# Kernel tuning notes

Measured on AMD Instinct MI355X. Metric: run time of the kernel, lower is better.

Reference implementation:

```python
import jax, jax.numpy as jnp
import numpy as np

B = 16384          # tokens
H = 2048           # hidden_size
E = 8              # num_experts
K = 2              # top-k
HF = H // 4        # expert bottleneck dim


def setup_inputs() -> dict:
    key = jax.random.key(0)
    k0, k1, k2, k3 = jax.random.split(key, 4)
    scale = lambda kk, shape, fan: jax.random.normal(kk, shape, jnp.float32) * (1.0 / np.sqrt(fan))
    x = jax.random.normal(k0, (B, H), jnp.float32)
    W1 = scale(k1, (E, H, HF), H)      # experts[e][0].weight (transposed)
    b1 = jnp.zeros((E, HF), jnp.float32)
    W2 = scale(k2, (E, HF), HF)        # experts[e][2].weight (out dim 1, no bias)
    Wg = scale(k3, (H, E), H)          # gate.weight (transposed)
    bg = jnp.zeros((E,), jnp.float32)
    return {"x": x, "W1": W1, "b1": b1, "W2": W2, "Wg": Wg, "bg": bg}


def reference(x, W1, b1, W2, Wg, bg):
    # Gating (eval mode: no noise branch)
    logits = x @ Wg + bg                                  # [B, E]
    top_w, top_i = jax.lax.top_k(logits, K)               # [B, K]
    w = jax.nn.softmax(top_w, axis=-1)                    # [B, K]
    # Scatter top-k softmax weights into dense combine weights [B, E];
    # unselected experts get weight 0, so the dense all-expert compute
    # below is mathematically identical to the masked dispatch loop.
    combine = jnp.zeros_like(logits).at[jnp.arange(x.shape[0])[:, None], top_i].add(w)
    # All-expert MLP: Linear -> exact GELU -> Linear(->1, no bias)
    h = jax.nn.gelu(jnp.einsum('bh,ehf->bef', x, W1) + b1, approximate=False)  # [B, E, HF]
    o = jnp.einsum('bef,ef->be', h, W2)                   # [B, E]
    final_scores = jnp.sum(combine * o, axis=-1, keepdims=True)  # [B, 1]
    return final_scores, logits
```

## Files before the change

### kernel.cpp

```cpp
#include <hip/hip_runtime.h>
#include <math.h>

#define B_TOK 16384
#define H_DIM 2048
#define NE    8
#define TOPK  2
#define HFD   512

#define BK 64
#define NKSTEP (H_DIM / BK)
#define PTMAX 129
#define PROWS 33792

static constexpr size_t OFF_COUNTS = 0;
static constexpr size_t OFF_CBASE  = 128;
static constexpr size_t OFF_BUCKET = 1024;
static constexpr size_t OFF_WSLOT  = 525312;
static constexpr size_t OFF_ROUTE  = 656384;
static constexpr size_t OFF_INV    = 721920;
static constexpr size_t OFF_WGT    = 1u << 20;
static constexpr size_t OFF_P4     = 1572864;
static constexpr size_t OFF_W1Q    = 4u << 20;
static constexpr size_t OFF_XB     = 20971520;

typedef short bfrag __attribute__((ext_vector_type(8)));
typedef float facc  __attribute__((ext_vector_type(16)));

__device__ inline unsigned short f2bf(float f) {
    union { float f; unsigned u; } v; v.f = f;
    unsigned r = v.u + 0x7FFFu + ((v.u >> 16) & 1u);
    return (unsigned short)(r >> 16);
}
__device__ inline unsigned pack2(float lo, float hi) {
    return (unsigned)f2bf(lo) | ((unsigned)f2bf(hi) << 16);
}

__device__ __forceinline__ void gload_lds16(const void* g, void* l) {
    __builtin_amdgcn_global_load_lds(
        (const __attribute__((address_space(1))) unsigned int*)g,
        (__attribute__((address_space(3))) unsigned int*)l, 16, 0, 0);
}

__global__ __launch_bounds__(256)
void wg_transpose_kernel(const float* __restrict__ Wg,
                         float* __restrict__ WgT)
{
    const int t = threadIdx.x;
    #pragma unroll
    for (int rep = 0; rep < H_DIM / 256; ++rep) {
        const int h = rep * 256 + t;
        const float4 a = *reinterpret_cast<const float4*>(Wg + (size_t)h * NE);
        const float4 b = *reinterpret_cast<const float4*>(Wg + (size_t)h * NE + 4);
        #pragma unroll
        for (int rr = 0; rr < 8; ++rr) {
            float* W = WgT + (size_t)rr * (NE * H_DIM);
            W[0 * H_DIM + h] = a.x;  W[1 * H_DIM + h] = a.y;
            W[2 * H_DIM + h] = a.z;  W[3 * H_DIM + h] = a.w;
            W[4 * H_DIM + h] = b.x;  W[5 * H_DIM + h] = b.y;
            W[6 * H_DIM + h] = b.z;  W[7 * H_DIM + h] = b.w;
        }
    }
}

__global__ __launch_bounds__(256)
void prep_w1_kernel(const float* __restrict__ W1,
                    unsigned short* __restrict__ W1q)
{
    const int e     = blockIdx.x >> 5;
    const int kstep = blockIdx.x & 31;
    const int tid   = threadIdx.x;

    const float* src = W1 + ((size_t)e * H_DIM + kstep * BK) * HFD;

    #pragma unroll
    for (int slot = 0; slot < 8; ++slot) {
        #pragma unroll
        for (int half = 0; half < 2; ++half) {
            const int f  = half * 256 + tid;
            const int fq = f >> 7;
            const int fl = f & 127;
            float v[8];
            #pragma unroll
            for (int j = 0; j < 8; ++j)
                v[j] = src[(size_t)(slot * 8 + j) * HFD + f];
            uint4 p;
            p.x = pack2(v[0], v[1]); p.y = pack2(v[2], v[3]);
            p.z = pack2(v[4], v[5]); p.w = pack2(v[6], v[7]);
            *reinterpret_cast<uint4*>(
                W1q + ((size_t)((e * 4 + fq) * 32 + kstep)) * 8192
                    + (slot * 128 + fl) * 8) = p;
        }
    }
}

__global__ __launch_bounds__(256)
void gate_logits_kernel(const float* __restrict__ x,
                        const float* __restrict__ WgT,
                        const float* __restrict__ bg,
                        float* __restrict__ out_logits,
                        float* __restrict__ wslot,
                        int*   __restrict__ route,
                        unsigned short* __restrict__ xb)
{
    __shared__ float Wlds[NE * H_DIM];

    const int tid = threadIdx.x;
    const float* Wsrc = WgT + (size_t)(blockIdx.x & 7) * (NE * H_DIM);
    #pragma unroll
    for (int i = 0; i < (NE * H_DIM) / (256 * 4); ++i) {
        const int idx = (i * 256 + tid) * 4;
        *reinterpret_cast<float4*>(&Wlds[idx]) =
            *reinterpret_cast<const float4*>(Wsrc + idx);
    }
    __syncthreads();

    const int w = tid >> 6, l = tid & 63;
    const int tbase = blockIdx.x * 64 + w * 16;

    for (int pass = 0; pass < 4; ++pass) {
        const int t0 = tbase + pass * 4;
        float acc[4][NE];
        #pragma unroll
        for (int j = 0; j < 4; ++j)
            #pragma unroll
            for (int e = 0; e < NE; ++e) acc[j][e] = 0.f;

        for (int i = 0; i < 8; ++i) {
            const int h = i * 256 + 4 * l;
            float4 xv[4];
            #pragma unroll
            for (int j = 0; j < 4; ++j)
                xv[j] = *reinterpret_cast<const float4*>(
                    x + (size_t)(t0 + j) * H_DIM + h);
            #pragma unroll
            for (int j = 0; j < 4; ++j) {
                uint2 pk;
                pk.x = pack2(xv[j].x, xv[j].y);
                pk.y = pack2(xv[j].z, xv[j].w);
                *reinterpret_cast<uint2*>(xb + (size_t)(t0 + j) * H_DIM + h) = pk;
            }
            #pragma unroll
            for (int e = 0; e < NE; ++e) {
                const float4 wv = *reinterpret_cast<const float4*>(&Wlds[e * H_DIM + h]);
                #pragma unroll
                for (int j = 0; j < 4; ++j)
                    acc[j][e] += xv[j].x * wv.x + xv[j].y * wv.y
                               + xv[j].z * wv.z + xv[j].w * wv.w;
            }
        }

        #pragma unroll
        for (int j = 0; j < 4; ++j)
            #pragma unroll
            for (int e = 0; e < NE; ++e)
                #pragma unroll
                for (int off = 32; off > 0; off >>= 1)
                    acc[j][e] += __shfl_xor(acc[j][e], off, 64);

        if (l == 0) {
            #pragma unroll
            for (int j = 0; j < 4; ++j) {
                const int tok = t0 + j;
                float lg[NE];
                #pragma unroll
                for (int e = 0; e < NE; ++e) lg[e] = acc[j][e] + bg[e];

                float4* lo = reinterpret_cast<float4*>(out_logits + (size_t)tok * NE);
                lo[0] = make_float4(lg[0], lg[1], lg[2], lg[3]);
                lo[1] = make_float4(lg[4], lg[5], lg[6], lg[7]);

                int i0 = 0; float v0 = lg[0];
                #pragma unroll
                for (int e = 1; e < NE; ++e)
                    if (lg[e] > v0) { v0 = lg[e]; i0 = e; }
                int i1 = -1; float v1 = -3.4e38f;
                #pragma unroll
                for (int e = 0; e < NE; ++e)
                    if (e != i0 && lg[e] > v1) { v1 = lg[e]; i1 = e; }

                const float w0 = 1.f / (1.f + expf(v1 - v0));
                wslot[tok * 2]     = w0;
                wslot[tok * 2 + 1] = 1.f - w0;
                route[tok] = i0 | (i1 << 8);
            }
        }
    }
}

__global__ __launch_bounds__(1024)
void route_kernel(const int* __restrict__ route,
                  int* __restrict__ counts,
                  int* __restrict__ bucket)
{
    __shared__ int lcnt[NE];
    __shared__ int lbase[NE];
    const int tid = threadIdx.x;
    const int tok = blockIdx.x * 1024 + tid;

    if (tid < NE) lcnt[tid] = 0;
    __syncthreads();

    const int rt = route[tok];
    const int i0 = rt & 255;
    const int i1 = rt >> 8;
    const int r0 = atomicAdd(&lcnt[i0], 1);
    const int r1 = atomicAdd(&lcnt[i1], 1);
    __syncthreads();

    if (tid < NE) lbase[tid] = atomicAdd(&counts[tid], lcnt[tid]);
    __syncthreads();

    bucket[i0 * B_TOK + lbase[i0] + r0] = tok * 2;
    bucket[i1 * B_TOK + lbase[i1] + r1] = tok * 2 + 1;
}

__global__ void prefix_kernel(const int* __restrict__ counts,
                              int* __restrict__ cbase)
{
    if (threadIdx.x == 0 && blockIdx.x == 0) {
        int acc = 0;
        for (int e = 0; e < NE; ++e) {
            const int cp = ((counts[e] + 127) >> 7) << 7;
            cbase[e]      = acc;
            cbase[NE + e] = cp;
            acc += cp;
        }
    }
}

__global__ __launch_bounds__(256)
void invfill_kernel(const int* __restrict__ bucket,
                    const int* __restrict__ counts,
                    const int* __restrict__ cbase,
                    int* __restrict__ inv)
{
    const int e   = blockIdx.x & 7;
    const int pos = (blockIdx.x >> 3) * 256 + threadIdx.x;
    if (pos < counts[e]) inv[bucket[e * B_TOK + pos]] = cbase[e] + pos;
}

__global__ __launch_bounds__(256, 4)
void expert_mfma_kernel(const unsigned short* __restrict__ xb,
                        const unsigned short* __restrict__ W1q,
                        const float* __restrict__ b1,
                        const float* __restrict__ W2,
                        const int* __restrict__ counts,
                        const int* __restrict__ cbase,
                        const int* __restrict__ bucket,
                        float* __restrict__ P4)
{
    const int e  = blockIdx.x & 7;
    const int r  = blockIdx.x >> 3;
    const int pt = r % PTMAX;
    const int fq = r / PTMAX;
    const int n  = counts[e];
    const int pos0 = pt * 128;
    if (pos0 >= n) return;
    const int nt = min(128, n - pos0);
    const int cb = cbase[e];

    __shared__ unsigned short Albs[8192];
    __shared__ unsigned short Blds[8192];
    __shared__ float o_part[2][128];

    const int tid = threadIdx.x;
    const int w   = tid >> 6;
    const int l   = tid & 63;
    const int lo5 = l & 31;
    const int hi  = l >> 5;
    const int wm  = w & 1;
    const int wn  = w >> 1;

    const unsigned short* Aimg = W1q + (size_t)((e * 4 + fq) * 32) * 8192;

    const unsigned short* xsrc0, *xsrc1, *xsrc2, *xsrc3;
    {
        const int u0 = 0 * 256 + tid, u1 = 1 * 256 + tid,
                  u2 = 2 * 256 + tid, u3 = 3 * 256 + tid;
        const int r0 = u0 >> 3, r1 = u1 >> 3, r2 = u2 >> 3, r3 = u3 >> 3;
        const int t0 = bucket[e * B_TOK + min(pos0 + r0, n - 1)] >> 1;
        const int t1 = bucket[e * B_TOK + min(pos0 + r1, n - 1)] >> 1;
        const int t2 = bucket[e * B_TOK + min(pos0 + r2, n - 1)] >> 1;
        const int t3 = bucket[e * B_TOK + min(pos0 + r3, n - 1)] >> 1;
        xsrc0 = xb + (size_t)t0 * H_DIM + (((u0 & 7) ^ (r0 & 7)) * 8);
        xsrc1 = xb + (size_t)t1 * H_DIM + (((u1 & 7) ^ (r1 & 7)) * 8);
        xsrc2 = xb + (size_t)t2 * H_DIM + (((u2 & 7) ^ (r2 & 7)) * 8);
        xsrc3 = xb + (size_t)t3 * H_DIM + (((u3 & 7) ^ (r3 & 7)) * 8);
    }

    facc acc00, acc01, acc10, acc11;
    #pragma unroll
    for (int q = 0; q < 16; ++q) {
        acc00[q] = 0.f; acc01[q] = 0.f; acc10[q] = 0.f; acc11[q] = 0.f;
    }

    for (int kk = 0; kk < NKSTEP; ++kk) {
        const unsigned short* as = Aimg + (size_t)kk * 8192;
        {
            const int o0 = (0 * 256 + tid) * 8, o1 = (1 * 256 + tid) * 8;
            const int o2 = (2 * 256 + tid) * 8, o3 = (3 * 256 + tid) * 8;
            gload_lds16(as + o0, Albs + o0);
            gload_lds16(as + o1, Albs + o1);
            gload_lds16(as + o2, Albs + o2);
            gload_lds16(as + o3, Albs + o3);
            gload_lds16(xsrc0 + kk * BK, Blds + o0);
            gload_lds16(xsrc1 + kk * BK, Blds + o1);
            gload_lds16(xsrc2 + kk * BK, Blds + o2);
            gload_lds16(xsrc3 + kk * BK, Blds + o3);
        }
        __syncthreads();

        #pragma unroll
        for (int s = 0; s < 4; ++s) {
            const int slot  = s * 2 + hi;
            const int chunk = slot ^ (lo5 & 7);
            const bfrag a0 = *reinterpret_cast<const bfrag*>(
                &Albs[(slot * 128 + wm * 64 + lo5) * 8]);
            const bfrag a1 = *reinterpret_cast<const bfrag*>(
                &Albs[(slot * 128 + wm * 64 + 32 + lo5) * 8]);
            const bfrag b0 = *reinterpret_cast<const bfrag*>(
                &Blds[((wn * 64 + lo5) * 8 + chunk) * 8]);
            const bfrag b1v = *reinterpret_cast<const bfrag*>(
                &Blds[((wn * 64 + 32 + lo5) * 8 + chunk) * 8]);
            acc00 = __builtin_amdgcn_mfma_f32_32x32x16_bf16(a0, b0,  acc00, 0, 0, 0);
            acc01 = __builtin_amdgcn_mfma_f32_32x32x16_bf16(a0, b1v, acc01, 0, 0, 0);
            acc10 = __builtin_amdgcn_mfma_f32_32x32x16_bf16(a1, b0,  acc10, 0, 0, 0);
            acc11 = __builtin_amdgcn_mfma_f32_32x32x16_bf16(a1, b1v, acc11, 0, 0, 0);
        }
        __syncthreads();
    }

    const float* b1e = b1 + e * HFD + fq * 128;
    const float* W2e = W2 + e * HFD + fq * 128;
    const float kInvSqrt2 = 0.70710678118654752f;

    float po0 = 0.f, po1 = 0.f;
    #pragma unroll
    for (int mb = 0; mb < 2; ++mb) {
        const int base = wm * 64 + mb * 32 + 4 * hi;
        #pragma unroll
        for (int q = 0; q < 16; ++q) {
            const int frow = base + (q & 3) + 8 * (q >> 2);
            const float bv = b1e[frow];
            const float wv = W2e[frow];
            const float h0 = (mb ? acc10[q] : acc00[q]) + bv;
            const float h1 = (mb ? acc11[q] : acc01[q]) + bv;
            po0 += 0.5f * h0 * (1.f + erff(h0 * kInvSqrt2)) * wv;
            po1 += 0.5f * h1 * (1.f + erff(h1 * kInvSqrt2)) * wv;
        }
    }
    po0 += __shfl_xor(po0, 32, 64);
    po1 += __shfl_xor(po1, 32, 64);

    if (hi == 0) {
        o_part[wm][wn * 64 + lo5]      = po0;
        o_part[wm][wn * 64 + 32 + lo5] = po1;
    }
    __syncthreads();

    if (tid < nt)
        P4[(size_t)fq * PROWS + cb + pos0 + tid] =
            o_part[0][tid] + o_part[1][tid];
}

__global__ __launch_bounds__(256)
void combine_kernel(const int* __restrict__ inv,
                    const float* __restrict__ P4,
                    const float* __restrict__ wslot,
                    float* __restrict__ out_scores)
{
    const int t = blockIdx.x * 256 + threadIdx.x;
    if (t >= B_TOK) return;
    const int g0 = inv[2 * t];
    const int g1 = inv[2 * t + 1];
    const float s0 = ((P4[g0] + P4[PROWS + g0]) + P4[2 * PROWS + g0])
                   + P4[3 * PROWS + g0];
    const float s1 = ((P4[g1] + P4[PROWS + g1]) + P4[2 * PROWS + g1])
                   + P4[3 * PROWS + g1];
    out_scores[t] = wslot[2 * t] * s0 + wslot[2 * t + 1] * s1;
}

extern "C" void kernel_launch(void* const* d_in, const int* in_sizes, int n_in,
                              void* d_out, int out_size, void* d_ws, size_t ws_size,
                              hipStream_t stream)
{
    const float* x  = (const float*)d_in[0];
    const float* W1 = (const float*)d_in[1];
    const float* b1 = (const float*)d_in[2];
    const float* W2 = (const float*)d_in[3];
    const float* Wg = (const float*)d_in[4];
    const float* bg = (const float*)d_in[5];

    float* out        = (float*)d_out;
    float* out_scores = out;
    float* out_logits = out + B_TOK;

    char* ws = (char*)d_ws;
    int*            counts = (int*)           (ws + OFF_COUNTS);
    int*            cbase  = (int*)           (ws + OFF_CBASE);
    int*            bucket = (int*)           (ws + OFF_BUCKET);
    float*          wslot  = (float*)         (ws + OFF_WSLOT);
    int*            route  = (int*)           (ws + OFF_ROUTE);
    int*            inv    = (int*)           (ws + OFF_INV);
    float*          WgT    = (float*)         (ws + OFF_WGT);
    float*          P4     = (float*)         (ws + OFF_P4);
    unsigned short* W1q    = (unsigned short*)(ws + OFF_W1Q);
    unsigned short* xb     = (unsigned short*)(ws + OFF_XB);

    hipMemsetAsync(counts, 0, NE * sizeof(int), stream);

    wg_transpose_kernel<<<1, 256, 0, stream>>>(Wg, WgT);

    prep_w1_kernel<<<NE * NKSTEP, 256, 0, stream>>>(W1, W1q);

    gate_logits_kernel<<<B_TOK / 64, 256, 0, stream>>>(x, WgT, bg, out_logits,
                                                       wslot, route, xb);

    route_kernel<<<B_TOK / 1024, 1024, 0, stream>>>(route, counts, bucket);

    prefix_kernel<<<1, 64, 0, stream>>>(counts, cbase);

    invfill_kernel<<<NE * (B_TOK / 256), 256, 0, stream>>>(bucket, counts,
                                                           cbase, inv);

    expert_mfma_kernel<<<NE * 4 * PTMAX, 256, 0, stream>>>(
        xb, W1q, b1, W2, counts, cbase, bucket, P4);

    combine_kernel<<<B_TOK / 256, 256, 0, stream>>>(inv, P4, wslot, out_scores);
}
```

Measured before the change: 250.7 us.

## Enlarge expert GEMM tiles to 256x256 with double-buffered LDS pipeline

The expert MFMA kernel moves from 128-token x 128-feature tiles with 256 threads to 256x256 tiles with 512 threads. The bottleneck dimension is now split into two halves instead of four. The K loop double-buffers A and B in LDS, prefetching the next step while computing the current one, and raises wave priority around the MFMA block. The W1 prep layout, padding to 256, the partial-sum buffer and the combine kernel are updated to match. This is meant to raise operand reuse per loaded byte, halve redundant gathers of x, and hide global-to-LDS latency. The cost is much higher LDS use (about 130KB) and register pressure, giving one block per CU and more padding waste on partial tiles.

Result: slower. 338.7 us (+35.1%).

```diff
diff --git a/kernel.cpp b/kernel.cpp
--- a/kernel.cpp
+++ b/kernel.cpp
@@ -9,8 +9,8 @@
 
 #define BK 64
 #define NKSTEP (H_DIM / BK)
-#define PTMAX 129
-#define PROWS 33792
+#define PT256 64
+#define PROWS 35840
 
 static constexpr size_t OFF_COUNTS = 0;
 static constexpr size_t OFF_CBASE  = 128;
@@ -19,8 +19,8 @@
 static constexpr size_t OFF_ROUTE  = 656384;
 static constexpr size_t OFF_INV    = 721920;
 static constexpr size_t OFF_WGT    = 1u << 20;
-static constexpr size_t OFF_P4     = 1572864;
-static constexpr size_t OFF_W1Q    = 4u << 20;
+static constexpr size_t OFF_P2     = 1572864;
+static constexpr size_t OFF_W1H    = 4u << 20;
 static constexpr size_t OFF_XB     = 20971520;
 
 typedef short bfrag __attribute__((ext_vector_type(8)));
@@ -64,7 +64,7 @@
 
 __global__ __launch_bounds__(256)
 void prep_w1_kernel(const float* __restrict__ W1,
-                    unsigned short* __restrict__ W1q)
+                    unsigned short* __restrict__ W1h)
 {
     const int e     = blockIdx.x >> 5;
     const int kstep = blockIdx.x & 31;
@@ -75,10 +75,8 @@
     #pragma unroll
     for (int slot = 0; slot < 8; ++slot) {
         #pragma unroll
-        for (int half = 0; half < 2; ++half) {
-            const int f  = half * 256 + tid;
-            const int fq = f >> 7;
-            const int fl = f & 127;
+        for (int fn = 0; fn < 2; ++fn) {
+            const int f = fn * 256 + tid;
             float v[8];
             #pragma unroll
             for (int j = 0; j < 8; ++j)
@@ -87,8 +85,8 @@
             p.x = pack2(v[0], v[1]); p.y = pack2(v[2], v[3]);
             p.z = pack2(v[4], v[5]); p.w = pack2(v[6], v[7]);
             *reinterpret_cast<uint4*>(
-                W1q + ((size_t)((e * 4 + fq) * 32 + kstep)) * 8192
-                    + (slot * 128 + fl) * 8) = p;
+                W1h + ((size_t)((e * 2 + fn) * 32 + kstep)) * 16384
+                    + (slot * 256 + tid) * 8) = p;
         }
     }
 }
@@ -220,7 +218,7 @@
     if (threadIdx.x == 0 && blockIdx.x == 0) {
         int acc = 0;
         for (int e = 0; e < NE; ++e) {
-            const int cp = ((counts[e] + 127) >> 7) << 7;
+            const int cp = ((counts[e] + 255) >> 8) << 8;
             cbase[e]      = acc;
             cbase[NE + e] = cp;
             acc += cp;
@@ -239,29 +237,29 @@
     if (pos < counts[e]) inv[bucket[e * B_TOK + pos]] = cbase[e] + pos;
 }
 
-__global__ __launch_bounds__(256, 4)
+__global__ __launch_bounds__(512, 1)
 void expert_mfma_kernel(const unsigned short* __restrict__ xb,
-                        const unsigned short* __restrict__ W1q,
+                        const unsigned short* __restrict__ W1h,
                         const float* __restrict__ b1,
                         const float* __restrict__ W2,
                         const int* __restrict__ counts,
                         const int* __restrict__ cbase,
                         const int* __restrict__ bucket,
-                        float* __restrict__ P4)
+                        float* __restrict__ P2)
 {
     const int e  = blockIdx.x & 7;
     const int r  = blockIdx.x >> 3;
-    const int pt = r % PTMAX;
-    const int fq = r / PTMAX;
+    const int fn = r & 1;
+    const int pt = r >> 1;
     const int n  = counts[e];
-    const int pos0 = pt * 128;
+    const int pos0 = pt * 256;
     if (pos0 >= n) return;
-    const int nt = min(128, n - pos0);
+    const int nt = min(256, n - pos0);
     const int cb = cbase[e];
 
-    __shared__ unsigned short Albs[8192];
-    __shared__ unsigned short Blds[8192];
-    __shared__ float o_part[2][128];
+    __shared__ unsigned short Ab[2][16384];
+    __shared__ unsigned short Bb[2][16384];
+    __shared__ float o_part[2][256];
 
     const int tid = threadIdx.x;
     const int w   = tid >> 6;
@@ -271,80 +269,95 @@
     const int wm  = w & 1;
     const int wn  = w >> 1;
 
-    const unsigned short* Aimg = W1q + (size_t)((e * 4 + fq) * 32) * 8192;
-
-    const unsigned short* xsrc0, *xsrc1, *xsrc2, *xsrc3;
-    {
-        const int u0 = 0 * 256 + tid, u1 = 1 * 256 + tid,
-                  u2 = 2 * 256 + tid, u3 = 3 * 256 + tid;
-        const int r0 = u0 >> 3, r1 = u1 >> 3, r2 = u2 >> 3, r3 = u3 >> 3;
-        const int t0 = bucket[e * B_TOK + min(pos0 + r0, n - 1)] >> 1;
-        const int t1 = bucket[e * B_TOK + min(pos0 + r1, n - 1)] >> 1;
-        const int t2 = bucket[e * B_TOK + min(pos0 + r2, n - 1)] >> 1;
-        const int t3 = bucket[e * B_TOK + min(pos0 + r3, n - 1)] >> 1;
-        xsrc0 = xb + (size_t)t0 * H_DIM + (((u0 & 7) ^ (r0 & 7)) * 8);
-        xsrc1 = xb + (size_t)t1 * H_DIM + (((u1 & 7) ^ (r1 & 7)) * 8);
-        xsrc2 = xb + (size_t)t2 * H_DIM + (((u2 & 7) ^ (r2 & 7)) * 8);
-        xsrc3 = xb + (size_t)t3 * H_DIM + (((u3 & 7) ^ (r3 & 7)) * 8);
-    }
-
-    facc acc00, acc01, acc10, acc11;
+    const unsigned short* Aimg = W1h + (size_t)((e * 2 + fn) * 32) * 16384;
+
+    const int u0 = 0 * 512 + tid, u1 = 1 * 512 + tid,
+              u2 = 2 * 512 + tid, u3 = 3 * 512 + tid;
+    const int r0 = u0 >> 3, r1 = u1 >> 3, r2 = u2 >> 3, r3 = u3 >> 3;
+    const int t0 = bucket[e * B_TOK + min(pos0 + r0, n - 1)] >> 1;
+    const int t1 = bucket[e * B_TOK + min(pos0 + r1, n - 1)] >> 1;
+    const int t2 = bucket[e * B_TOK + min(pos0 + r2, n - 1)] >> 1;
+    const int t3 = bucket[e * B_TOK + min(pos0 + r3, n - 1)] >> 1;
+    const unsigned short* xs0 = xb + (size_t)t0 * H_DIM + (((u0 & 7) ^ (r0 & 7)) * 8);
+    const unsigned short* xs1 = xb + (size_t)t1 * H_DIM + (((u1 & 7) ^ (r1 & 7)) * 8);
+    const unsigned short* xs2 = xb + (size_t)t2 * H_DIM + (((u2 & 7) ^ (r2 & 7)) * 8);
+    const unsigned short* xs3 = xb + (size_t)t3 * H_DIM + (((u3 & 7) ^ (r3 & 7)) * 8);
+    const int o0 = u0 * 8, o1 = u1 * 8, o2 = u2 * 8, o3 = u3 * 8;
+
+    facc acc[4][2];
     #pragma unroll
-    for (int q = 0; q < 16; ++q) {
-        acc00[q] = 0.f; acc01[q] = 0.f; acc10[q] = 0.f; acc11[q] = 0.f;
-    }
+    for (int m = 0; m < 4; ++m)
+        #pragma unroll
+        for (int nb = 0; nb < 2; ++nb)
+            #pragma unroll
+            for (int q = 0; q < 16; ++q) acc[m][nb][q] = 0.f;
+
+    #define STAGE(KK, BUF) do {                                                \
+        const unsigned short* as_ = Aimg + (size_t)(KK) * 16384;               \
+        gload_lds16(as_ + o0, &Ab[BUF][o0]);                                   \
+        gload_lds16(as_ + o1, &Ab[BUF][o1]);                                   \
+        gload_lds16(as_ + o2, &Ab[BUF][o2]);                                   \
+        gload_lds16(as_ + o3, &Ab[BUF][o3]);                                   \
+        gload_lds16(xs0 + (KK) * BK, &Bb[BUF][o0]);                            \
+        gload_lds16(xs1 + (KK) * BK, &Bb[BUF][o1]);                            \
+        gload_lds16(xs2 + (KK) * BK, &Bb[BUF][o2]);                            \
+        gload_lds16(xs3 + (KK) * BK, &Bb[BUF][o3]);                            \
+    } while (0)
+
+    #define COMPUTE(BUF) do {                                                  \
+        _Pragma("unroll")                                                      \
+        for (int ks = 0; ks < 4; ++ks) {                                       \
+            const int slot = ks * 2 + hi;                                      \
+            bfrag a[4], bb[2];                                                 \
+            _Pragma("unroll")                                                  \
+            for (int m = 0; m < 4; ++m)                                        \
+                a[m] = *reinterpret_cast<const bfrag*>(                        \
+                    &Ab[BUF][(slot * 256 + wm * 128 + m * 32 + lo5) * 8]);     \
+            _Pragma("unroll")                                                  \
+            for (int nb = 0; nb < 2; ++nb) {                                   \
+                const int row = wn * 64 + nb * 32 + lo5;                       \
+                const int ch  = slot ^ (row & 7);                              \
+                bb[nb] = *reinterpret_cast<const bfrag*>(                      \
+                    &Bb[BUF][(row * 8 + ch) * 8]);                             \
+            }                                                                  \
+            _Pragma("unroll")                                                  \
+            for (int m = 0; m < 4; ++m)                                        \
+                _Pragma("unroll")                                              \
+                for (int nb = 0; nb < 2; ++nb)                                 \
+                    acc[m][nb] = __builtin_amdgcn_mfma_f32_32x32x16_bf16(      \
+                        a[m], bb[nb], acc[m][nb], 0, 0, 0);                    \
+        }                                                                      \
+    } while (0)
+
+    STAGE(0, 0);
+    __syncthreads();
 
     for (int kk = 0; kk < NKSTEP; ++kk) {
-        const unsigned short* as = Aimg + (size_t)kk * 8192;
-        {
-            const int o0 = (0 * 256 + tid) * 8, o1 = (1 * 256 + tid) * 8;
-            const int o2 = (2 * 256 + tid) * 8, o3 = (3 * 256 + tid) * 8;
-            gload_lds16(as + o0, Albs + o0);
-            gload_lds16(as + o1, Albs + o1);
-            gload_lds16(as + o2, Albs + o2);
-            gload_lds16(as + o3, Albs + o3);
-            gload_lds16(xsrc0 + kk * BK, Blds + o0);
-            gload_lds16(xsrc1 + kk * BK, Blds + o1);
-            gload_lds16(xsrc2 + kk * BK, Blds + o2);
-            gload_lds16(xsrc3 + kk * BK, Blds + o3);
-        }
+        const int cur = kk & 1;
+        if (kk + 1 < NKSTEP) STAGE(kk + 1, cur ^ 1);
+        __builtin_amdgcn_s_setprio(1);
+        COMPUTE(cur);
+        __builtin_amdgcn_s_setprio(0);
         __syncthreads();
-
-        #pragma unroll
-        for (int s = 0; s < 4; ++s) {
-            const int slot  = s * 2 + hi;
-            const int chunk = slot ^ (lo5 & 7);
-            const bfrag a0 = *reinterpret_cast<const bfrag*>(
-                &Albs[(slot * 128 + wm * 64 + lo5) * 8]);
-            const bfrag a1 = *reinterpret_cast<const bfrag*>(
-                &Albs[(slot * 128 + wm * 64 + 32 + lo5) * 8]);
-            const bfrag b0 = *reinterpret_cast<const bfrag*>(
-                &Blds[((wn * 64 + lo5) * 8 + chunk) * 8]);
-            const bfrag b1v = *reinterpret_cast<const bfrag*>(
-                &Blds[((wn * 64 + 32 + lo5) * 8 + chunk) * 8]);
-            acc00 = __builtin_amdgcn_mfma_f32_32x32x16_bf16(a0, b0,  acc00, 0, 0, 0);
-            acc01 = __builtin_amdgcn_mfma_f32_32x32x16_bf16(a0, b1v, acc01, 0, 0, 0);
-            acc10 = __builtin_amdgcn_mfma_f32_32x32x16_bf16(a1, b0,  acc10, 0, 0, 0);
-            acc11 = __builtin_amdgcn_mfma_f32_32x32x16_bf16(a1, b1v, acc11, 0, 0, 0);
-        }
-        __syncthreads();
-    }
-
-    const float* b1e = b1 + e * HFD + fq * 128;
-    const float* W2e = W2 + e * HFD + fq * 128;
+    }
+    #undef STAGE
+    #undef COMPUTE
+
+    const float* b1e = b1 + e * HFD + fn * 256;
+    const float* W2e = W2 + e * HFD + fn * 256;
     const float kInvSqrt2 = 0.70710678118654752f;
 
     float po0 = 0.f, po1 = 0.f;
     #pragma unroll
-    for (int mb = 0; mb < 2; ++mb) {
-        const int base = wm * 64 + mb * 32 + 4 * hi;
+    for (int m = 0; m < 4; ++m) {
+        const int base = wm * 128 + m * 32 + 4 * hi;
         #pragma unroll
         for (int q = 0; q < 16; ++q) {
             const int frow = base + (q & 3) + 8 * (q >> 2);
             const float bv = b1e[frow];
             const float wv = W2e[frow];
-            const float h0 = (mb ? acc10[q] : acc00[q]) + bv;
-            const float h1 = (mb ? acc11[q] : acc01[q]) + bv;
+            const float h0 = acc[m][0][q] + bv;
+            const float h1 = acc[m][1][q] + bv;
             po0 += 0.5f * h0 * (1.f + erff(h0 * kInvSqrt2)) * wv;
             po1 += 0.5f * h1 * (1.f + erff(h1 * kInvSqrt2)) * wv;
         }
@@ -359,13 +372,13 @@
     __syncthreads();
 
     if (tid < nt)
-        P4[(size_t)fq * PROWS + cb + pos0 + tid] =
+        P2[(size_t)fn * PROWS + cb + pos0 + tid] =
             o_part[0][tid] + o_part[1][tid];
 }
 
 __global__ __launch_bounds__(256)
 void combine_kernel(const int* __restrict__ inv,
-                    const float* __restrict__ P4,
+                    const float* __restrict__ P2,
                     const float* __restrict__ wslot,
                     float* __restrict__ out_scores)
 {
@@ -373,10 +386,8 @@
     if (t >= B_TOK) return;
     const int g0 = inv[2 * t];
     const int g1 = inv[2 * t + 1];
-    const float s0 = ((P4[g0] + P4[PROWS + g0]) + P4[2 * PROWS + g0])
-                   + P4[3 * PROWS + g0];
-    const float s1 = ((P4[g1] + P4[PROWS + g1]) + P4[2 * PROWS + g1])
-                   + P4[3 * PROWS + g1];
+    const float s0 = P2[g0] + P2[PROWS + g0];
+    const float s1 = P2[g1] + P2[PROWS + g1];
     out_scores[t] = wslot[2 * t] * s0 + wslot[2 * t + 1] * s1;
 }
 
@@ -403,15 +414,15 @@
     int*            route  = (int*)           (ws + OFF_ROUTE);
     int*            inv    = (int*)           (ws + OFF_INV);
     float*          WgT    = (float*)         (ws + OFF_WGT);
-    float*          P4     = (float*)         (ws + OFF_P4);
-    unsigned short* W1q    = (unsigned short*)(ws + OFF_W1Q);
+    float*          P2     = (float*)         (ws + OFF_P2);
+    unsigned short* W1h    = (unsigned short*)(ws + OFF_W1H);
     unsigned short* xb     = (unsigned short*)(ws + OFF_XB);
 
     hipMemsetAsync(counts, 0, NE * sizeof(int), stream);
 
     wg_transpose_kernel<<<1, 256, 0, stream>>>(Wg, WgT);
 
-    prep_w1_kernel<<<NE * NKSTEP, 256, 0, stream>>>(W1, W1q);
+    prep_w1_kernel<<<NE * NKSTEP, 256, 0, stream>>>(W1, W1h);
 
     gate_logits_kernel<<<B_TOK / 64, 256, 0, stream>>>(x, WgT, bg, out_logits,
                                                        wslot, route, xb);
@@ -423,8 +434,8 @@
     invfill_kernel<<<NE * (B_TOK / 256), 256, 0, stream>>>(bucket, counts,
                                                            cbase, inv);
 
-    expert_mfma_kernel<<<NE * 4 * PTMAX, 256, 0, stream>>>(
-        xb, W1q, b1, W2, counts, cbase, bucket, P4);
-
-    combine_kernel<<<B_TOK / 256, 256, 0, stream>>>(inv, P4, wslot, out_scores);
-}
+    expert_mfma_kernel<<<NE * 2 * PT256, 512, 0, stream>>>(
+        xb, W1h, b1, W2, counts, cbase, bucket, P2);
+
+    combine_kernel<<<B_TOK / 256, 256, 0, stream>>>(inv, P2, wslot, out_scores);
+}
```

## Retile expert GEMM to 256 features by 64 tokens with BK=32

Applied to the files above, without the earlier changes.

Restructures the expert MFMA kernel's tile. Each block now covers 256 hidden features (half of HF) by 64 tokens, instead of 128 features by 128 tokens, and uses a K-step of 32. W1 is repacked to match, and the partial-output buffer drops from 4 feature slices to 2, so the combine step sums fewer partials. The aim is to cut how often the gathered token rows are re-read across feature slices and to get finer load balance over the variable per-expert token counts. In exchange, each W1 tile is reused across fewer tokens and there are twice as many k-iterations, each with a barrier.

Result: slower. 266.1 us (+6.1%).

```diff
diff --git a/kernel.cpp b/kernel.cpp
--- a/kernel.cpp
+++ b/kernel.cpp
@@ -7,9 +7,9 @@
 #define TOPK  2
 #define HFD   512
 
-#define BK 64
+#define BK 32
 #define NKSTEP (H_DIM / BK)
-#define PTMAX 129
+#define PT64  256
 #define PROWS 33792
 
 static constexpr size_t OFF_COUNTS = 0;
@@ -19,8 +19,8 @@
 static constexpr size_t OFF_ROUTE  = 656384;
 static constexpr size_t OFF_INV    = 721920;
 static constexpr size_t OFF_WGT    = 1u << 20;
-static constexpr size_t OFF_P4     = 1572864;
-static constexpr size_t OFF_W1Q    = 4u << 20;
+static constexpr size_t OFF_P2     = 1572864;
+static constexpr size_t OFF_W1H    = 4u << 20;
 static constexpr size_t OFF_XB     = 20971520;
 
 typedef short bfrag __attribute__((ext_vector_type(8)));
@@ -64,31 +64,29 @@
 
 __global__ __launch_bounds__(256)
 void prep_w1_kernel(const float* __restrict__ W1,
-                    unsigned short* __restrict__ W1q)
-{
-    const int e     = blockIdx.x >> 5;
-    const int kstep = blockIdx.x & 31;
+                    unsigned short* __restrict__ W1h)
+{
+    const int e     = blockIdx.x >> 6;
+    const int kstep = blockIdx.x & 63;
     const int tid   = threadIdx.x;
 
     const float* src = W1 + ((size_t)e * H_DIM + kstep * BK) * HFD;
 
     #pragma unroll
-    for (int slot = 0; slot < 8; ++slot) {
-        #pragma unroll
-        for (int half = 0; half < 2; ++half) {
-            const int f  = half * 256 + tid;
-            const int fq = f >> 7;
-            const int fl = f & 127;
+    for (int s = 0; s < 4; ++s) {
+        #pragma unroll
+        for (int fh = 0; fh < 2; ++fh) {
+            const int f = fh * 256 + tid;
             float v[8];
             #pragma unroll
             for (int j = 0; j < 8; ++j)
-                v[j] = src[(size_t)(slot * 8 + j) * HFD + f];
+                v[j] = src[(size_t)(s * 8 + j) * HFD + f];
             uint4 p;
             p.x = pack2(v[0], v[1]); p.y = pack2(v[2], v[3]);
             p.z = pack2(v[4], v[5]); p.w = pack2(v[6], v[7]);
             *reinterpret_cast<uint4*>(
-                W1q + ((size_t)((e * 4 + fq) * 32 + kstep)) * 8192
-                    + (slot * 128 + fl) * 8) = p;
+                W1h + ((size_t)((e * 2 + fh) * 64 + kstep)) * 8192
+                    + (s * 256 + tid) * 8) = p;
         }
     }
 }
@@ -241,52 +239,41 @@
 
 __global__ __launch_bounds__(256, 4)
 void expert_mfma_kernel(const unsigned short* __restrict__ xb,
-                        const unsigned short* __restrict__ W1q,
+                        const unsigned short* __restrict__ W1h,
                         const float* __restrict__ b1,
                         const float* __restrict__ W2,
                         const int* __restrict__ counts,
                         const int* __restrict__ cbase,
                         const int* __restrict__ bucket,
-                        float* __restrict__ P4)
+                        float* __restrict__ P2)
 {
     const int e  = blockIdx.x & 7;
     const int r  = blockIdx.x >> 3;
-    const int pt = r % PTMAX;
-    const int fq = r / PTMAX;
+    const int fh = r & 1;
+    const int pt = r >> 1;
     const int n  = counts[e];
-    const int pos0 = pt * 128;
+    const int pos0 = pt * 64;
     if (pos0 >= n) return;
-    const int nt = min(128, n - pos0);
+    const int nt = min(64, n - pos0);
     const int cb = cbase[e];
 
-    __shared__ unsigned short Albs[8192];
-    __shared__ unsigned short Blds[8192];
-    __shared__ float o_part[2][128];
+    __shared__ unsigned short Ab[8192];
+    __shared__ unsigned short Bb[2048];
+    __shared__ float o_part[4][64];
 
     const int tid = threadIdx.x;
-    const int w   = tid >> 6;
+    const int fg  = tid >> 6;
     const int l   = tid & 63;
     const int lo5 = l & 31;
     const int hi  = l >> 5;
-    const int wm  = w & 1;
-    const int wn  = w >> 1;
-
-    const unsigned short* Aimg = W1q + (size_t)((e * 4 + fq) * 32) * 8192;
-
-    const unsigned short* xsrc0, *xsrc1, *xsrc2, *xsrc3;
-    {
-        const int u0 = 0 * 256 + tid, u1 = 1 * 256 + tid,
-                  u2 = 2 * 256 + tid, u3 = 3 * 256 + tid;
-        const int r0 = u0 >> 3, r1 = u1 >> 3, r2 = u2 >> 3, r3 = u3 >> 3;
-        const int t0 = bucket[e * B_TOK + min(pos0 + r0, n - 1)] >> 1;
-        const int t1 = bucket[e * B_TOK + min(pos0 + r1, n - 1)] >> 1;
-        const int t2 = bucket[e * B_TOK + min(pos0 + r2, n - 1)] >> 1;
-        const int t3 = bucket[e * B_TOK + min(pos0 + r3, n - 1)] >> 1;
-        xsrc0 = xb + (size_t)t0 * H_DIM + (((u0 & 7) ^ (r0 & 7)) * 8);
-        xsrc1 = xb + (size_t)t1 * H_DIM + (((u1 & 7) ^ (r1 & 7)) * 8);
-        xsrc2 = xb + (size_t)t2 * H_DIM + (((u2 & 7) ^ (r2 & 7)) * 8);
-        xsrc3 = xb + (size_t)t3 * H_DIM + (((u3 & 7) ^ (r3 & 7)) * 8);
-    }
+
+    const unsigned short* Aimg = W1h + (size_t)((e * 2 + fh) * 64) * 8192;
+
+    const int brow = tid >> 2;
+    const int bc   = tid & 3;
+    const int btok = bucket[e * B_TOK + min(pos0 + brow, n - 1)] >> 1;
+    const unsigned short* bsrc = xb + (size_t)btok * H_DIM + ((bc ^ (brow & 3)) * 8);
+    const int bo = tid * 8;
 
     facc acc00, acc01, acc10, acc11;
     #pragma unroll
@@ -294,34 +281,31 @@
         acc00[q] = 0.f; acc01[q] = 0.f; acc10[q] = 0.f; acc11[q] = 0.f;
     }
 
+    const int o0 = tid * 8, o1 = (256 + tid) * 8,
+              o2 = (512 + tid) * 8, o3 = (768 + tid) * 8;
+
     for (int kk = 0; kk < NKSTEP; ++kk) {
         const unsigned short* as = Aimg + (size_t)kk * 8192;
-        {
-            const int o0 = (0 * 256 + tid) * 8, o1 = (1 * 256 + tid) * 8;
-            const int o2 = (2 * 256 + tid) * 8, o3 = (3 * 256 + tid) * 8;
-            gload_lds16(as + o0, Albs + o0);
-            gload_lds16(as + o1, Albs + o1);
-            gload_lds16(as + o2, Albs + o2);
-            gload_lds16(as + o3, Albs + o3);
-            gload_lds16(xsrc0 + kk * BK, Blds + o0);
-            gload_lds16(xsrc1 + kk * BK, Blds + o1);
-            gload_lds16(xsrc2 + kk * BK, Blds + o2);
-            gload_lds16(xsrc3 + kk * BK, Blds + o3);
-        }
+        gload_lds16(as + o0, Ab + o0);
+        gload_lds16(as + o1, Ab + o1);
+        gload_lds16(as + o2, Ab + o2);
+        gload_lds16(as + o3, Ab + o3);
+        gload_lds16(bsrc + kk * BK, Bb + bo);
         __syncthreads();
 
         #pragma unroll
-        for (int s = 0; s < 4; ++s) {
-            const int slot  = s * 2 + hi;
-            const int chunk = slot ^ (lo5 & 7);
+        for (int ks = 0; ks < 2; ++ks) {
+            const int slot = ks * 2 + hi;
             const bfrag a0 = *reinterpret_cast<const bfrag*>(
-                &Albs[(slot * 128 + wm * 64 + lo5) * 8]);
+                &Ab[(slot * 256 + fg * 64 + lo5) * 8]);
             const bfrag a1 = *reinterpret_cast<const bfrag*>(
-                &Albs[(slot * 128 + wm * 64 + 32 + lo5) * 8]);
-            const bfrag b0 = *reinterpret_cast<const bfrag*>(
-                &Blds[((wn * 64 + lo5) * 8 + chunk) * 8]);
+                &Ab[(slot * 256 + fg * 64 + 32 + lo5) * 8]);
+            const int row0 = lo5,      c0 = slot ^ (row0 & 3);
+            const int row1 = 32 + lo5, c1 = slot ^ (row1 & 3);
+            const bfrag b0  = *reinterpret_cast<const bfrag*>(
+                &Bb[(row0 * 4 + c0) * 8]);
             const bfrag b1v = *reinterpret_cast<const bfrag*>(
-                &Blds[((wn * 64 + 32 + lo5) * 8 + chunk) * 8]);
+                &Bb[(row1 * 4 + c1) * 8]);
             acc00 = __builtin_amdgcn_mfma_f32_32x32x16_bf16(a0, b0,  acc00, 0, 0, 0);
             acc01 = __builtin_amdgcn_mfma_f32_32x32x16_bf16(a0, b1v, acc01, 0, 0, 0);
             acc10 = __builtin_amdgcn_mfma_f32_32x32x16_bf16(a1, b0,  acc10, 0, 0, 0);
@@ -330,21 +314,21 @@
         __syncthreads();
     }
 
-    const float* b1e = b1 + e * HFD + fq * 128;
-    const float* W2e = W2 + e * HFD + fq * 128;
+    const float* b1e = b1 + e * HFD + fh * 256 + fg * 64;
+    const float* W2e = W2 + e * HFD + fh * 256 + fg * 64;
     const float kInvSqrt2 = 0.70710678118654752f;
 
     float po0 = 0.f, po1 = 0.f;
     #pragma unroll
-    for (int mb = 0; mb < 2; ++mb) {
-        const int base = wm * 64 + mb * 32 + 4 * hi;
+    for (int m = 0; m < 2; ++m) {
+        const int base = m * 32 + 4 * hi;
         #pragma unroll
         for (int q = 0; q < 16; ++q) {
             const int frow = base + (q & 3) + 8 * (q >> 2);
             const float bv = b1e[frow];
             const float wv = W2e[frow];
-            const float h0 = (mb ? acc10[q] : acc00[q]) + bv;
-            const float h1 = (mb ? acc11[q] : acc01[q]) + bv;
+            const float h0 = (m ? acc10[q] : acc00[q]) + bv;
+            const float h1 = (m ? acc11[q] : acc01[q]) + bv;
             po0 += 0.5f * h0 * (1.f + erff(h0 * kInvSqrt2)) * wv;
             po1 += 0.5f * h1 * (1.f + erff(h1 * kInvSqrt2)) * wv;
         }
@@ -353,19 +337,20 @@
     po1 += __shfl_xor(po1, 32, 64);
 
     if (hi == 0) {
-        o_part[wm][wn * 64 + lo5]      = po0;
-        o_part[wm][wn * 64 + 32 + lo5] = po1;
+        o_part[fg][lo5]      = po0;
+        o_part[fg][32 + lo5] = po1;
     }
     __syncthreads();
 
     if (tid < nt)
-        P4[(size_t)fq * PROWS + cb + pos0 + tid] =
-            o_part[0][tid] + o_part[1][tid];
+        P2[(size_t)fh * PROWS + cb + pos0 + tid] =
+            (o_part[0][tid] + o_part[1][tid])
+          + (o_part[2][tid] + o_part[3][tid]);
 }
 
 __global__ __launch_bounds__(256)
 void combine_kernel(const int* __restrict__ inv,
-                    const float* __restrict__ P4,
+                    const float* __restrict__ P2,
                     const float* __restrict__ wslot,
                     float* __restrict__ out_scores)
 {
@@ -373,10 +358,8 @@
     if (t >= B_TOK) return;
     const int g0 = inv[2 * t];
     const int g1 = inv[2 * t + 1];
-    const float s0 = ((P4[g0] + P4[PROWS + g0]) + P4[2 * PROWS + g0])
-                   + P4[3 * PROWS + g0];
-    const float s1 = ((P4[g1] + P4[PROWS + g1]) + P4[2 * PROWS + g1])
-                   + P4[3 * PROWS + g1];
+    const float s0 = P2[g0] + P2[PROWS + g0];
+    const float s1 = P2[g1] + P2[PROWS + g1];
     out_scores[t] = wslot[2 * t] * s0 + wslot[2 * t + 1] * s1;
 }
 
@@ -403,15 +386,15 @@
     int*            route  = (int*)           (ws + OFF_ROUTE);
     int*            inv    = (int*)           (ws + OFF_INV);
     float*          WgT    = (float*)         (ws + OFF_WGT);
-    float*          P4     = (float*)         (ws + OFF_P4);
-    unsigned short* W1q    = (unsigned short*)(ws + OFF_W1Q);
+    float*          P2     = (float*)         (ws + OFF_P2);
+    unsigned short* W1h    = (unsigned short*)(ws + OFF_W1H);
     unsigned short* xb     = (unsigned short*)(ws + OFF_XB);
 
     hipMemsetAsync(counts, 0, NE * sizeof(int), stream);
 
     wg_transpose_kernel<<<1, 256, 0, stream>>>(Wg, WgT);
 
-    prep_w1_kernel<<<NE * NKSTEP, 256, 0, stream>>>(W1, W1q);
+    prep_w1_kernel<<<NE * NKSTEP, 256, 0, stream>>>(W1, W1h);
 
     gate_logits_kernel<<<B_TOK / 64, 256, 0, stream>>>(x, WgT, bg, out_logits,
                                                        wslot, route, xb);
@@ -423,8 +406,8 @@
     invfill_kernel<<<NE * (B_TOK / 256), 256, 0, stream>>>(bucket, counts,
                                                            cbase, inv);
 
-    expert_mfma_kernel<<<NE * 4 * PTMAX, 256, 0, stream>>>(
-        xb, W1q, b1, W2, counts, cbase, bucket, P4);
-
-    combine_kernel<<<B_TOK / 256, 256, 0, stream>>>(inv, P4, wslot, out_scores);
-}
+    expert_mfma_kernel<<<NE * 2 * PT64, 256, 0, stream>>>(
+        xb, W1h, b1, W2, counts, cbase, bucket, P2);
+
+    combine_kernel<<<B_TOK / 256, 256, 0, stream>>>(inv, P2, wslot, out_scores);
+}
```
